# Kernel optimization log

Hardware: AMD Instinct MI355X
Metric: run time of the kernel (lower is better)

The kernel has to match this reference:

```python
import jax, jax.numpy as jnp
import numpy as np

D = 1024
H = 16
DH = D // H  # 64
EPS = 1e-6


def setup_inputs() -> dict:
    key = jax.random.key(0)
    ks = jax.random.split(key, 12)
    B, Nq, Nk = 4, 2048, 2048
    s = 1.0 / np.sqrt(D)
    return {
        "x": jax.random.normal(ks[0], (B, Nq, D), dtype=jnp.float32),
        "context": jax.random.normal(ks[1], (B, Nk, D), dtype=jnp.float32),
        "Wq": jax.random.normal(ks[2], (D, D), dtype=jnp.float32) * s,
        "bq": jnp.zeros((D,), dtype=jnp.float32),
        "Wk": jax.random.normal(ks[3], (D, D), dtype=jnp.float32) * s,
        "bk": jnp.zeros((D,), dtype=jnp.float32),
        "Wv": jax.random.normal(ks[4], (D, D), dtype=jnp.float32) * s,
        "bv": jnp.zeros((D,), dtype=jnp.float32),
        "Wo": jax.random.normal(ks[5], (D, D), dtype=jnp.float32) * s,
        "bo": jnp.zeros((D,), dtype=jnp.float32),
    }


def _split_heads(t):
    B, N, _ = t.shape
    return t.reshape(B, N, H, DH).transpose(0, 2, 1, 3)  # (B,H,N,DH)


def reference(x, context, Wq, bq, Wk, bk, Wv, bv, Wo, bo):
    B, Nq, _ = x.shape
    # QKV projections (torch Linear: x @ W.T + b)
    q = _split_heads(x @ Wq.T + bq)          # (B,H,Nq,DH)
    k = _split_heads(context @ Wk.T + bk)    # (B,H,Nk,DH)
    v = _split_heads(context @ Wv.T + bv)    # (B,H,Nk,DH)
    # QK-norm (use_qk_norm=True), scale buffer = 1.0
    q = q / (jnp.linalg.norm(q, axis=-1, keepdims=True) + EPS)
    k = k / (jnp.linalg.norm(k, axis=-1, keepdims=True) + EPS)
    scale = jnp.float32(1.0)
    attn = jnp.einsum("bhqd,bhkd->bhqk", q, k) * scale
    attn = jax.nn.softmax(attn, axis=-1)
    out = jnp.einsum("bhqk,bhkd->bhqd", attn, v)  # (B,H,Nq,DH)
    out = out.transpose(0, 2, 1, 3).reshape(B, Nq, D)
    return out @ Wo.T + bo
```

## Files before the change

kernel.cpp:

```cpp
#include <hip/hip_runtime.h>

typedef unsigned short u16;
typedef unsigned int u32;
typedef __attribute__((ext_vector_type(8))) short bf16x8;
typedef __attribute__((ext_vector_type(4))) float f32x4;
typedef __attribute__((ext_vector_type(16))) float f32x16;
typedef __attribute__((ext_vector_type(4))) u32 u32x4;

#define D_MODEL 1024
#define NHEAD 16
#define DHEAD 64
#define SEQ 2048
#define BATCH 4
#define MTOT (BATCH * SEQ)

#define MFMA16(A, B, C) __builtin_amdgcn_mfma_f32_16x16x32_bf16((A), (B), (C), 0, 0, 0)
#define MFMA32(A, B, C) __builtin_amdgcn_mfma_f32_32x32x16_bf16((A), (B), (C), 0, 0, 0)

__device__ __forceinline__ u16 f2bf(float f) {
  u32 u = __builtin_bit_cast(u32, f);
  u = (u + 0x7FFFu + ((u >> 16) & 1u)) >> 16;
  return (u16)u;
}
__device__ __forceinline__ float bf2f(u16 h) {
  u32 u = ((u32)h) << 16;
  return __builtin_bit_cast(float, u);
}

__device__ __forceinline__ void async_copy16(void* lds, const void* g) {
  __builtin_amdgcn_global_load_lds(
      (const __attribute__((address_space(1))) u32*)g,
      (__attribute__((address_space(3))) u32*)lds, 16, 0, 0);
}

__device__ __forceinline__ u32 cvtpk_bf16(float lo, float hi) {
  u32 r;
  asm("v_cvt_pk_bf16_f32 %0, %1, %2" : "=v"(r) : "v"(lo), "v"(hi));
  return r;
}
__device__ __forceinline__ void permswap(u32& a, u32& b) {
  asm("v_permlane32_swap_b32 %0, %1" : "+v"(a), "+v"(b));
}

__global__ void cvt_f32_bf16(const float* __restrict__ s, u16* __restrict__ d, int n4) {
  int i = blockIdx.x * blockDim.x + threadIdx.x;
  int st = gridDim.x * blockDim.x;
  for (; i < n4; i += st) {
    float4 v = ((const float4*)s)[i];
    ushort4 o;
    o.x = f2bf(v.x); o.y = f2bf(v.y); o.z = f2bf(v.z); o.w = f2bf(v.w);
    ((ushort4*)d)[i] = o;
  }
}

#define BM 128
#define BN 128
#define BKG 64

template <int SM>
__global__ __launch_bounds__(256, 2) void gemm_bt(const u16* __restrict__ A,
                                                  const u16* __restrict__ Bw,
                                                  const float* __restrict__ bias,
                                                  void* __restrict__ Cout,
                                                  int M, int N, int K) {
  __shared__ u16 As[BM * BKG];
  __shared__ u16 Bs[BN * BKG];
  const int tid = threadIdx.x;
  const int l = tid & 63;
  const int wid = tid >> 6;
  const int nwg = gridDim.x;
  const int bid = blockIdx.x;
  const int cpx = nwg >> 3;
  const int swz = (bid & 7) * cpx + (bid >> 3);
  const int ntile = N / BN;
  const int m0 = (swz / ntile) * BM;
  const int n0 = (swz % ntile) * BN;
  const int wr = wid >> 1, wc = wid & 1;
  const int r = l & 15, kg = l >> 4;
  f32x4 acc[4][4] = {};
  char* AsB = (char*)As;
  char* BsB = (char*)Bs;
  const int arow = l >> 3;
  const int agran = (l & 7) ^ arow;

  for (int kt = 0; kt < K; kt += BKG) {
#pragma unroll
    for (int cc = 0; cc < 4; ++cc) {
      int c = wid + (cc << 2);
      int rowi = (c << 3) + arow;
      const char* ga = (const char*)A + ((size_t)(m0 + rowi) * K + kt) * 2 + agran * 16;
      async_copy16(AsB + c * 1024, ga);
      const char* gb = (const char*)Bw + ((size_t)(n0 + rowi) * K + kt) * 2 + agran * 16;
      async_copy16(BsB + c * 1024, gb);
    }
    __syncthreads();
#pragma unroll
    for (int half = 0; half < 2; ++half) {
      const int g = ((half << 2) + kg) ^ (r & 7);
      bf16x8 af[4], bf[4];
#pragma unroll
      for (int i = 0; i < 4; ++i) {
        af[i] = *(const bf16x8*)(AsB + (wr * 64 + i * 16 + r) * 128 + g * 16);
        bf[i] = *(const bf16x8*)(BsB + (wc * 64 + i * 16 + r) * 128 + g * 16);
      }
#pragma unroll
      for (int i = 0; i < 4; ++i)
#pragma unroll
        for (int j = 0; j < 4; ++j)
          acc[i][j] = MFMA16(af[i], bf[j], acc[i][j]);
    }
    __syncthreads();
  }

  if (SM == 3) {
    u16* C = (u16*)Cout;
    float bvj[4];
#pragma unroll
    for (int j = 0; j < 4; ++j) bvj[j] = bias[n0 + wc * 64 + j * 16 + r];
#pragma unroll
    for (int i = 0; i < 4; ++i) {
      const int row0 = m0 + wr * 64 + i * 16 + kg * 4;
#pragma unroll
      for (int jj = 0; jj < 4; ++jj) {
        float t[4];
        float s2 = 0.f;
#pragma unroll
        for (int j = 0; j < 4; ++j) {
          t[j] = acc[i][j][jj] + bvj[j];
          s2 += t[j] * t[j];
        }
        s2 += __shfl_xor(s2, 1);
        s2 += __shfl_xor(s2, 2);
        s2 += __shfl_xor(s2, 4);
        s2 += __shfl_xor(s2, 8);
        const float inv = 1.0f / (sqrtf(s2) + 1e-6f);
#pragma unroll
        for (int j = 0; j < 4; ++j)
          C[(size_t)(row0 + jj) * N + n0 + wc * 64 + j * 16 + r] = f2bf(t[j] * inv);
      }
    }
    return;
  }

#pragma unroll
  for (int i = 0; i < 4; ++i) {
#pragma unroll
    for (int j = 0; j < 4; ++j) {
      const int col = n0 + wc * 64 + j * 16 + r;
      const float bv = bias[col];
      const int row0 = m0 + wr * 64 + i * 16 + kg * 4;
      if (SM == 1) {
        float* C = (float*)Cout;
#pragma unroll
        for (int jj = 0; jj < 4; ++jj)
          C[(size_t)(row0 + jj) * N + col] = acc[i][j][jj] + bv;
      } else {
        u16* C = (u16*)Cout;
        const int hh = col >> 6, dh = col & 63;
        const int bb = row0 >> 11, tok = row0 & 2047;
        ushort4 o;
        o.x = f2bf(acc[i][j][0] + bv);
        o.y = f2bf(acc[i][j][1] + bv);
        o.z = f2bf(acc[i][j][2] + bv);
        o.w = f2bf(acc[i][j][3] + bv);
        *(ushort4*)(C + ((size_t)((bb * 16 + hh) * 64 + dh) * SEQ + tok)) = o;
      }
    }
  }
}

#define KVB 64
#define NT (SEQ / KVB)

__global__ __launch_bounds__(256, 4) void attn_kernel(const u16* __restrict__ Q,
                                                      const u16* __restrict__ K,
                                                      const u16* __restrict__ Vt,
                                                      u16* __restrict__ O) {
  __shared__ alignas(16) u16 Ks[2][KVB * 64];
  __shared__ alignas(16) u16 Vs[2][64 * KVB];
  const int tid = threadIdx.x;
  const int l = tid & 63;
  const int wid = tid >> 6;
  const int qg = l & 31;
  const int half = l >> 5;
  const int bid = blockIdx.x;
  const int swz = (bid & 7) * 128 + (bid >> 3);
  const int qt = swz & 15;
  const int bh = swz >> 4;
  const int b = bh >> 4, h = bh & 15;

  bf16x8 qf[4];
  {
    const u16* q0 = Q + ((size_t)(b * SEQ + qt * 128 + wid * 32 + qg)) * D_MODEL + h * 64 + half * 8;
#pragma unroll
    for (int dc = 0; dc < 4; ++dc) qf[dc] = *(const bf16x8*)(q0 + dc * 16);
  }
  f32x16 oacc[2] = {};
  float lrun = 0.f;

  auto stage = [&](int bufi, int t) {
    const int kv0 = t * KVB;
    char* KsB = (char*)Ks[bufi];
    char* VsB = (char*)Vs[bufi];
    const int rowin = l >> 3;
    const int slot = l & 7;
#pragma unroll
    for (int cc = 0; cc < 4; ++cc) {
      int c = wid + (cc << 2);
      if (c < 8) {
        int row = (c << 3) + rowin;
        int q = slot ^ ((row ^ (row >> 3)) & 7);
        const char* g = (const char*)K +
                        ((size_t)(b * SEQ + kv0 + row) * D_MODEL + h * 64 + q * 8) * 2;
        async_copy16(KsB + c * 1024, g);
      } else {
        int row = ((c - 8) << 3) + rowin;
        int q = slot ^ ((row ^ (row >> 3)) & 7);
        const char* g = (const char*)Vt +
                        ((size_t)(bh * 64 + row) * SEQ + kv0 + q * 8) * 2;
        async_copy16(VsB + (c - 8) * 1024, g);
      }
    }
  };

  stage(0, 0);
  __syncthreads();
  int buf = 0;

  for (int t = 0; t < NT; ++t) {
    if (t + 1 < NT) stage(buf ^ 1, t + 1);
    const char* KsB = (const char*)Ks[buf];
    const char* VsB = (const char*)Vs[buf];

    f32x16 st[2] = {};
    __builtin_amdgcn_s_setprio(1);
#pragma unroll
    for (int t32 = 0; t32 < 2; ++t32) {
      const int rowK = t32 * 32 + qg;
      const int swk = (rowK ^ (rowK >> 3)) & 7;
#pragma unroll
      for (int dc = 0; dc < 4; ++dc) {
        const int p = (dc * 2 + half) ^ swk;
        bf16x8 kf = *(const bf16x8*)(KsB + rowK * 128 + p * 16);
        st[t32] = MFMA32(kf, qf[dc], st[t32]);
      }
    }
    __builtin_amdgcn_s_setprio(0);

    float rs = 0.f;
#pragma unroll
    for (int t32 = 0; t32 < 2; ++t32)
#pragma unroll
      for (int rr = 0; rr < 16; ++rr) {
        float z = __builtin_fmaf(st[t32][rr], 1.4426950408889634f, -1.4426950408889634f);
        float pv = __builtin_amdgcn_exp2f(z);
        st[t32][rr] = pv;
        rs += pv;
      }
    lrun += rs;

#pragma unroll
    for (int t32 = 0; t32 < 2; ++t32) {
#pragma unroll
      for (int cc = 0; cc < 2; ++cc) {
        const int base = cc * 8;
        u32 wA = cvtpk_bf16(st[t32][base + 0], st[t32][base + 1]);
        u32 wB = cvtpk_bf16(st[t32][base + 2], st[t32][base + 3]);
        u32 wC = cvtpk_bf16(st[t32][base + 4], st[t32][base + 5]);
        u32 wD = cvtpk_bf16(st[t32][base + 6], st[t32][base + 7]);
        permswap(wA, wC);
        permswap(wB, wD);
        u32x4 pw = {wA, wB, wC, wD};
        bf16x8 pf = __builtin_bit_cast(bf16x8, pw);
        const int qw = ((t32 * 2 + cc) << 1) + half;
        __builtin_amdgcn_s_setprio(1);
#pragma unroll
        for (int dt = 0; dt < 2; ++dt) {
          const int rowV = dt * 32 + qg;
          const int pp = qw ^ ((rowV ^ (rowV >> 3)) & 7);
          bf16x8 vf = *(const bf16x8*)(VsB + rowV * 128 + pp * 16);
          oacc[dt] = MFMA32(vf, pf, oacc[dt]);
        }
        __builtin_amdgcn_s_setprio(0);
      }
    }
    __syncthreads();
    buf ^= 1;
  }

  lrun += __shfl_xor(lrun, 32);
  const float inv = 1.0f / lrun;
  u32* orow = (u32*)(O + ((size_t)(b * SEQ + qt * 128 + wid * 32 + qg)) * D_MODEL + h * 64);
#pragma unroll
  for (int dt = 0; dt < 2; ++dt)
#pragma unroll
    for (int w = 0; w < 8; ++w) {
      const int dh = dt * 32 + (w & 1) * 2 + 8 * (w >> 1) + 4 * half;
      u32 pk = cvtpk_bf16(oacc[dt][2 * w] * inv, oacc[dt][2 * w + 1] * inv);
      orow[dh >> 1] = pk;
    }
}

extern "C" void kernel_launch(void* const* d_in, const int* in_sizes, int n_in,
                              void* d_out, int out_size, void* d_ws, size_t ws_size,
                              hipStream_t stream) {
  const float* x   = (const float*)d_in[0];
  const float* ctx = (const float*)d_in[1];
  const float* Wq  = (const float*)d_in[2];
  const float* bq  = (const float*)d_in[3];
  const float* Wk  = (const float*)d_in[4];
  const float* bk  = (const float*)d_in[5];
  const float* Wv  = (const float*)d_in[6];
  const float* bv  = (const float*)d_in[7];
  const float* Wo  = (const float*)d_in[8];
  const float* bo  = (const float*)d_in[9];
  float* out = (float*)d_out;

  const size_t NTOK = (size_t)MTOT * D_MODEL;
  const size_t WSZ = (size_t)D_MODEL * D_MODEL;
  u16* xb  = (u16*)d_ws;
  u16* cb  = xb + NTOK;
  u16* wqb = cb + NTOK;
  u16* wkb = wqb + WSZ;
  u16* wvb = wkb + WSZ;
  u16* wob = wvb + WSZ;
  u16* Qb  = wob + WSZ;
  u16* Kb  = Qb + NTOK;
  u16* Vtb = Kb + NTOK;
  (void)in_sizes; (void)n_in; (void)out_size; (void)ws_size;

  dim3 blk(256);
  cvt_f32_bf16<<<2048, blk, 0, stream>>>(x, xb, (int)(NTOK / 4));
  cvt_f32_bf16<<<2048, blk, 0, stream>>>(ctx, cb, (int)(NTOK / 4));
  cvt_f32_bf16<<<512, blk, 0, stream>>>(Wq, wqb, (int)(WSZ / 4));
  cvt_f32_bf16<<<512, blk, 0, stream>>>(Wk, wkb, (int)(WSZ / 4));
  cvt_f32_bf16<<<512, blk, 0, stream>>>(Wv, wvb, (int)(WSZ / 4));
  cvt_f32_bf16<<<512, blk, 0, stream>>>(Wo, wob, (int)(WSZ / 4));

  gemm_bt<3><<<512, blk, 0, stream>>>(xb, wqb, bq, Qb, MTOT, D_MODEL, D_MODEL);
  gemm_bt<3><<<512, blk, 0, stream>>>(cb, wkb, bk, Kb, MTOT, D_MODEL, D_MODEL);
  gemm_bt<2><<<512, blk, 0, stream>>>(cb, wvb, bv, Vtb, MTOT, D_MODEL, D_MODEL);

  attn_kernel<<<1024, blk, 0, stream>>>(Qb, Kb, Vtb, xb);

  gemm_bt<1><<<512, blk, 0, stream>>>(xb, wob, bo, out, MTOT, D_MODEL, D_MODEL);
}
```

Before: 213.1 us.

## Fold log2e into Q norm, merge conversion launches, simplify attention staging loop

The log2(e) factor moves into the Q-normalization epilogue of the projection GEMM, so the attention softmax calls exp2 directly with no per-score FMA. The constant max-offset is dropped, which relies on normalized scores staying bounded. The six f32-to-bf16 conversion launches are merged into three two-tensor kernels to cut launch overhead. In the attention kernel, staging uses precomputed, incrementing global pointers and a manually unrolled two-buffer loop, which removes per-iteration index math and buffer selection. The row sum is split into four partial accumulators.

```diff
diff --git a/kernel.cpp b/kernel.cpp
--- a/kernel.cpp
+++ b/kernel.cpp
@@ -13,6 +13,7 @@
 #define SEQ 2048
 #define BATCH 4
 #define MTOT (BATCH * SEQ)
+#define LOG2E 1.4426950408889634f
 
 #define MFMA16(A, B, C) __builtin_amdgcn_mfma_f32_16x16x32_bf16((A), (B), (C), 0, 0, 0)
 #define MFMA32(A, B, C) __builtin_amdgcn_mfma_f32_32x32x16_bf16((A), (B), (C), 0, 0, 0)
@@ -22,10 +23,6 @@
   u = (u + 0x7FFFu + ((u >> 16) & 1u)) >> 16;
   return (u16)u;
 }
-__device__ __forceinline__ float bf2f(u16 h) {
-  u32 u = ((u32)h) << 16;
-  return __builtin_bit_cast(float, u);
-}
 
 __device__ __forceinline__ void async_copy16(void* lds, const void* g) {
   __builtin_amdgcn_global_load_lds(
@@ -42,14 +39,18 @@
   asm("v_permlane32_swap_b32 %0, %1" : "+v"(a), "+v"(b));
 }
 
-__global__ void cvt_f32_bf16(const float* __restrict__ s, u16* __restrict__ d, int n4) {
+__global__ void cvt2(const float* __restrict__ s0, u16* __restrict__ d0,
+                     const float* __restrict__ s1, u16* __restrict__ d1, int n4) {
   int i = blockIdx.x * blockDim.x + threadIdx.x;
   int st = gridDim.x * blockDim.x;
-  for (; i < n4; i += st) {
-    float4 v = ((const float4*)s)[i];
+  for (; i < 2 * n4; i += st) {
+    const float* s = (i < n4) ? s0 : s1;
+    u16* d = (i < n4) ? d0 : d1;
+    int j = (i < n4) ? i : (i - n4);
+    float4 v = ((const float4*)s)[j];
     ushort4 o;
     o.x = f2bf(v.x); o.y = f2bf(v.y); o.z = f2bf(v.z); o.w = f2bf(v.w);
-    ((ushort4*)d)[i] = o;
+    ((ushort4*)d)[j] = o;
   }
 }
 
@@ -62,7 +63,7 @@
                                                   const u16* __restrict__ Bw,
                                                   const float* __restrict__ bias,
                                                   void* __restrict__ Cout,
-                                                  int M, int N, int K) {
+                                                  int M, int N, int K, float sMul) {
   __shared__ u16 As[BM * BKG];
   __shared__ u16 Bs[BN * BKG];
   const int tid = threadIdx.x;
@@ -133,7 +134,7 @@
         s2 += __shfl_xor(s2, 2);
         s2 += __shfl_xor(s2, 4);
         s2 += __shfl_xor(s2, 8);
-        const float inv = 1.0f / (sqrtf(s2) + 1e-6f);
+        const float inv = sMul / (sqrtf(s2) + 1e-6f);
 #pragma unroll
         for (int j = 0; j < 4; ++j)
           C[(size_t)(row0 + jj) * N + n0 + wc * 64 + j * 16 + r] = f2bf(t[j] * inv);
@@ -176,8 +177,8 @@
                                                       const u16* __restrict__ K,
                                                       const u16* __restrict__ Vt,
                                                       u16* __restrict__ O) {
-  __shared__ alignas(16) u16 Ks[2][KVB * 64];
-  __shared__ alignas(16) u16 Vs[2][64 * KVB];
+  __shared__ alignas(16) u16 KsA[KVB * 64], KsB[KVB * 64];
+  __shared__ alignas(16) u16 VsA[64 * KVB], VsB[64 * KVB];
   const int tid = threadIdx.x;
   const int l = tid & 63;
   const int wid = tid >> 6;
@@ -189,75 +190,76 @@
   const int bh = swz >> 4;
   const int b = bh >> 4, h = bh & 15;
 
+  const int srow = l >> 3, slot = l & 7;
+  const int r0 = (wid << 3) + srow;
+  const int r1 = ((wid + 4) << 3) + srow;
+  const int sw0 = (r0 ^ (r0 >> 3)) & 7;
+  const int sw1 = (r1 ^ (r1 >> 3)) & 7;
+  const u16* pK0 = K + ((size_t)(b * SEQ) + r0) * D_MODEL + h * 64 + (slot ^ sw0) * 8;
+  const u16* pK1 = K + ((size_t)(b * SEQ) + r1) * D_MODEL + h * 64 + (slot ^ sw1) * 8;
+  const u16* pV0 = Vt + ((size_t)(bh * 64) + r0) * SEQ + (slot ^ sw0) * 8;
+  const u16* pV1 = Vt + ((size_t)(bh * 64) + r1) * SEQ + (slot ^ sw1) * 8;
+  const int ldsc0 = wid * 1024, ldsc1 = (wid + 4) * 1024;
+
   bf16x8 qf[4];
   {
     const u16* q0 = Q + ((size_t)(b * SEQ + qt * 128 + wid * 32 + qg)) * D_MODEL + h * 64 + half * 8;
 #pragma unroll
     for (int dc = 0; dc < 4; ++dc) qf[dc] = *(const bf16x8*)(q0 + dc * 16);
   }
+  float z0 = 0.f;
+  asm volatile("" : "+v"(z0));
+  f32x16 zc;
+#pragma unroll
+  for (int i = 0; i < 16; ++i) zc[i] = z0;
+
   f32x16 oacc[2] = {};
   float lrun = 0.f;
 
-  auto stage = [&](int bufi, int t) {
-    const int kv0 = t * KVB;
-    char* KsB = (char*)Ks[bufi];
-    char* VsB = (char*)Vs[bufi];
-    const int rowin = l >> 3;
-    const int slot = l & 7;
-#pragma unroll
-    for (int cc = 0; cc < 4; ++cc) {
-      int c = wid + (cc << 2);
-      if (c < 8) {
-        int row = (c << 3) + rowin;
-        int q = slot ^ ((row ^ (row >> 3)) & 7);
-        const char* g = (const char*)K +
-                        ((size_t)(b * SEQ + kv0 + row) * D_MODEL + h * 64 + q * 8) * 2;
-        async_copy16(KsB + c * 1024, g);
-      } else {
-        int row = ((c - 8) << 3) + rowin;
-        int q = slot ^ ((row ^ (row >> 3)) & 7);
-        const char* g = (const char*)Vt +
-                        ((size_t)(bh * 64 + row) * SEQ + kv0 + q * 8) * 2;
-        async_copy16(VsB + (c - 8) * 1024, g);
-      }
-    }
+  auto stage = [&](u16* KsX, u16* VsX) {
+    async_copy16((char*)KsX + ldsc0, pK0);
+    async_copy16((char*)KsX + ldsc1, pK1);
+    async_copy16((char*)VsX + ldsc0, pV0);
+    async_copy16((char*)VsX + ldsc1, pV1);
+    pK0 += (size_t)KVB * D_MODEL;
+    pK1 += (size_t)KVB * D_MODEL;
+    pV0 += KVB;
+    pV1 += KVB;
   };
 
-  stage(0, 0);
-  __syncthreads();
-  int buf = 0;
-
-  for (int t = 0; t < NT; ++t) {
-    if (t + 1 < NT) stage(buf ^ 1, t + 1);
-    const char* KsB = (const char*)Ks[buf];
-    const char* VsB = (const char*)Vs[buf];
-
-    f32x16 st[2] = {};
+  auto process = [&](const u16* KsX, const u16* VsX) {
+    const char* KsC = (const char*)KsX;
+    const char* VsC = (const char*)VsX;
+    f32x16 st[2];
     __builtin_amdgcn_s_setprio(1);
 #pragma unroll
     for (int t32 = 0; t32 < 2; ++t32) {
       const int rowK = t32 * 32 + qg;
       const int swk = (rowK ^ (rowK >> 3)) & 7;
-#pragma unroll
-      for (int dc = 0; dc < 4; ++dc) {
-        const int p = (dc * 2 + half) ^ swk;
-        bf16x8 kf = *(const bf16x8*)(KsB + rowK * 128 + p * 16);
+      bf16x8 kf0 = *(const bf16x8*)(KsC + rowK * 128 + (half ^ swk) * 16);
+      st[t32] = MFMA32(kf0, qf[0], zc);
+#pragma unroll
+      for (int dc = 1; dc < 4; ++dc) {
+        bf16x8 kf = *(const bf16x8*)(KsC + rowK * 128 + ((dc * 2 + half) ^ swk) * 16);
         st[t32] = MFMA32(kf, qf[dc], st[t32]);
       }
     }
     __builtin_amdgcn_s_setprio(0);
 
-    float rs = 0.f;
+    float rs0 = 0.f, rs1 = 0.f, rs2 = 0.f, rs3 = 0.f;
 #pragma unroll
     for (int t32 = 0; t32 < 2; ++t32)
 #pragma unroll
-      for (int rr = 0; rr < 16; ++rr) {
-        float z = __builtin_fmaf(st[t32][rr], 1.4426950408889634f, -1.4426950408889634f);
-        float pv = __builtin_amdgcn_exp2f(z);
-        st[t32][rr] = pv;
-        rs += pv;
-      }
-    lrun += rs;
+      for (int rr = 0; rr < 16; rr += 4) {
+        float p0 = __builtin_amdgcn_exp2f(st[t32][rr + 0]);
+        float p1 = __builtin_amdgcn_exp2f(st[t32][rr + 1]);
+        float p2 = __builtin_amdgcn_exp2f(st[t32][rr + 2]);
+        float p3 = __builtin_amdgcn_exp2f(st[t32][rr + 3]);
+        st[t32][rr + 0] = p0; st[t32][rr + 1] = p1;
+        st[t32][rr + 2] = p2; st[t32][rr + 3] = p3;
+        rs0 += p0; rs1 += p1; rs2 += p2; rs3 += p3;
+      }
+    lrun += (rs0 + rs1) + (rs2 + rs3);
 
 #pragma unroll
     for (int t32 = 0; t32 < 2; ++t32) {
@@ -278,14 +280,23 @@
         for (int dt = 0; dt < 2; ++dt) {
           const int rowV = dt * 32 + qg;
           const int pp = qw ^ ((rowV ^ (rowV >> 3)) & 7);
-          bf16x8 vf = *(const bf16x8*)(VsB + rowV * 128 + pp * 16);
+          bf16x8 vf = *(const bf16x8*)(VsC + rowV * 128 + pp * 16);
           oacc[dt] = MFMA32(vf, pf, oacc[dt]);
         }
         __builtin_amdgcn_s_setprio(0);
       }
     }
+  };
+
+  stage(KsA, VsA);
+  __syncthreads();
+  for (int t = 0; t < NT; t += 2) {
+    stage(KsB, VsB);
+    process(KsA, VsA);
     __syncthreads();
-    buf ^= 1;
+    if (t + 2 < NT) stage(KsA, VsA);
+    process(KsB, VsB);
+    __syncthreads();
   }
 
   lrun += __shfl_xor(lrun, 32);
@@ -330,18 +341,15 @@
   (void)in_sizes; (void)n_in; (void)out_size; (void)ws_size;
 
   dim3 blk(256);
-  cvt_f32_bf16<<<2048, blk, 0, stream>>>(x, xb, (int)(NTOK / 4));
-  cvt_f32_bf16<<<2048, blk, 0, stream>>>(ctx, cb, (int)(NTOK / 4));
-  cvt_f32_bf16<<<512, blk, 0, stream>>>(Wq, wqb, (int)(WSZ / 4));
-  cvt_f32_bf16<<<512, blk, 0, stream>>>(Wk, wkb, (int)(WSZ / 4));
-  cvt_f32_bf16<<<512, blk, 0, stream>>>(Wv, wvb, (int)(WSZ / 4));
-  cvt_f32_bf16<<<512, blk, 0, stream>>>(Wo, wob, (int)(WSZ / 4));
-
-  gemm_bt<3><<<512, blk, 0, stream>>>(xb, wqb, bq, Qb, MTOT, D_MODEL, D_MODEL);
-  gemm_bt<3><<<512, blk, 0, stream>>>(cb, wkb, bk, Kb, MTOT, D_MODEL, D_MODEL);
-  gemm_bt<2><<<512, blk, 0, stream>>>(cb, wvb, bv, Vtb, MTOT, D_MODEL, D_MODEL);
+  cvt2<<<2048, blk, 0, stream>>>(x, xb, ctx, cb, (int)(NTOK / 4));
+  cvt2<<<512, blk, 0, stream>>>(Wq, wqb, Wk, wkb, (int)(WSZ / 4));
+  cvt2<<<512, blk, 0, stream>>>(Wv, wvb, Wo, wob, (int)(WSZ / 4));
+
+  gemm_bt<3><<<512, blk, 0, stream>>>(xb, wqb, bq, Qb, MTOT, D_MODEL, D_MODEL, LOG2E);
+  gemm_bt<3><<<512, blk, 0, stream>>>(cb, wkb, bk, Kb, MTOT, D_MODEL, D_MODEL, 1.0f);
+  gemm_bt<2><<<512, blk, 0, stream>>>(cb, wvb, bv, Vtb, MTOT, D_MODEL, D_MODEL, 0.f);
 
   attn_kernel<<<1024, blk, 0, stream>>>(Qb, Kb, Vtb, xb);
 
-  gemm_bt<1><<<512, blk, 0, stream>>>(xb, wob, bo, out, MTOT, D_MODEL, D_MODEL);
-}
+  gemm_bt<1><<<512, blk, 0, stream>>>(xb, wob, bo, out, MTOT, D_MODEL, D_MODEL, 0.f);
+}
```

Measured after the change: 266.3 us. 1.25x slower.
